# Kernel tuning notes

Hardware: AMD Instinct MI355X
Metric: run time of the kernel (lower is better)

## Reference

```python
import jax, jax.numpy as jnp
import numpy as np

EPS = 1e-5
K = 20
THRESH = 0.5

def _bn_relu(x, g, b, m, v):
    # eval-mode BatchNorm1d followed by ReLU
    return jax.nn.relu(g * (x - m) * jax.lax.rsqrt(v + EPS) + b)

def setup_inputs() -> dict:
    key = jax.random.key(0)
    ks = jax.random.split(key, 16)
    T, C, CI, E, NC = 16384, 256, 8, 5, 13
    B, N = 2, T // 2
    inp = {
        "f_sem": jax.random.normal(ks[0], (T, C), jnp.float32),
        "f_ins": jax.random.normal(ks[1], (T, CI), jnp.float32),
        # equal-size, sorted batch assignment (2 clouds of 8192 points)
        "batch": jnp.repeat(jnp.arange(B, dtype=jnp.int64), N),
        # semantic_adaptation_fc: Linear(C,C) + BN + ReLU
        "W_sem": jax.random.normal(ks[2], (C, C), jnp.float32) * (1.0 / np.sqrt(C)),
        "b_sem": jnp.zeros((C,), jnp.float32),
        "g_sem": jnp.ones((C,), jnp.float32),
        "beta_sem": jnp.zeros((C,), jnp.float32),
        "m_sem": jax.random.normal(ks[3], (C,), jnp.float32) * 0.1,
        "v_sem": jax.random.uniform(ks[4], (C,), jnp.float32, 0.5, 1.5),
        # inst_fc: Linear(8,C) + BN + ReLU
        "W_ins": jax.random.normal(ks[5], (CI, C), jnp.float32) * (1.0 / np.sqrt(CI)),
        "b_ins": jnp.zeros((C,), jnp.float32),
        "g_ins": jnp.ones((C,), jnp.float32),
        "beta_ins": jnp.zeros((C,), jnp.float32),
        "m_ins": jax.random.normal(ks[6], (C,), jnp.float32) * 0.1,
        "v_ins": jax.random.uniform(ks[7], (C,), jnp.float32, 0.5, 1.5),
        # instance_embedding_fc: plain Linear(C,E)
        "W_emb": jax.random.normal(ks[8], (C, E), jnp.float32) * (1.0 / np.sqrt(C)),
        "b_emb": jnp.zeros((E,), jnp.float32),
        # classifier_fc: plain Linear(C,NC)
        "W_cls": jax.random.normal(ks[9], (C, NC), jnp.float32) * (1.0 / np.sqrt(C)),
        "b_cls": jnp.zeros((NC,), jnp.float32),
    }
    return inp

def _instance_fusion(e_ins, f_sem, batch):
    # assumes sorted batch with equal-size segments (enforced by setup_inputs)
    T, C = f_sem.shape
    B = int(batch[-1]) + 1
    N = T // B
    e = e_ins.reshape(B, N, -1)
    f = f_sem.reshape(B, N, C)
    # squared Euclidean pairwise distances per cloud: [B, N, N]
    sq = jnp.sum(e * e, axis=-1)
    d2 = sq[:, :, None] + sq[:, None, :] - 2.0 * jnp.einsum("bnd,bmd->bnm", e, e)
    d2 = jnp.maximum(d2, 0.0)
    neg_vals, idx = jax.lax.top_k(-d2, K)          # k smallest distances, [B,N,K]
    within = (-neg_vals) <= THRESH * THRESH        # distance <= threshold
    self_idx = jnp.broadcast_to(jnp.arange(N)[None, :, None], idx.shape)
    col = jnp.where(within, idx, self_idx)         # fall back to self outside threshold
    neigh = jax.vmap(lambda fb, cb: fb[cb])(f, col)  # [B,N,K,C]
    return jnp.max(neigh, axis=2).reshape(T, C)      # scatter-max == max over neighbors

def reference(f_sem, f_ins, batch,
              W_sem, b_sem, g_sem, beta_sem, m_sem, v_sem,
              W_ins, b_ins, g_ins, beta_ins, m_ins, v_ins,
              W_emb, b_emb, W_cls, b_cls):
    f_sem_prime = _bn_relu(f_sem @ W_sem + b_sem, g_sem, beta_sem, m_sem, v_sem)
    f_ins_h = _bn_relu(f_ins @ W_ins + b_ins, g_ins, beta_ins, m_ins, v_ins)
    f_sins = f_ins_h + f_sem_prime
    e_ins = f_sins @ W_emb + b_emb
    f_isem = _instance_fusion(e_ins, f_sem, batch)
    p_sem = f_isem @ W_cls + b_cls
    return (p_sem, e_ins)
```

## Files before the change

kernel.cpp:

```cpp
#include <hip/hip_runtime.h>
#include <math.h>

#define T 16384
#define C 256
#define CI 8
#define EDIM 5
#define NC 13
#define NPTS 8192
#define KNN 20
#define CAP 192
#define FR 32
#define FRPB 8
#define NCVT 256

typedef float f4v __attribute__((ext_vector_type(4)));
typedef _Float16 h8 __attribute__((ext_vector_type(8)));
typedef _Float16 h4v __attribute__((ext_vector_type(4)));

__global__ __launch_bounds__(256) void front_kernel(
    const float* __restrict__ f_sem, const float* __restrict__ f_ins,
    const float* __restrict__ W_sem, const float* __restrict__ b_sem,
    const float* __restrict__ g_sem, const float* __restrict__ beta_sem,
    const float* __restrict__ m_sem, const float* __restrict__ v_sem,
    const float* __restrict__ W_ins, const float* __restrict__ b_ins,
    const float* __restrict__ g_ins, const float* __restrict__ beta_ins,
    const float* __restrict__ m_ins, const float* __restrict__ v_ins,
    const float* __restrict__ W_emb, const float* __restrict__ b_emb,
    float* __restrict__ eA, double* __restrict__ eD,
    float* __restrict__ out_e, _Float16* __restrict__ fsem_h)
{
    const int nFront = T / FR;
    if (blockIdx.x >= nFront) {
        const size_t total = (size_t)T * C;
        const size_t stride = (size_t)NCVT * 256 * 8;
        size_t i = ((size_t)(blockIdx.x - nFront) * 256 + threadIdx.x) * 8;
        for (; i < total; i += stride) {
            const float4 a = *(const float4*)(f_sem + i);
            const float4 b = *(const float4*)(f_sem + i + 4);
            h8 h;
            h[0] = (_Float16)a.x; h[1] = (_Float16)a.y;
            h[2] = (_Float16)a.z; h[3] = (_Float16)a.w;
            h[4] = (_Float16)b.x; h[5] = (_Float16)b.y;
            h[6] = (_Float16)b.z; h[7] = (_Float16)b.w;
            *(h8*)(fsem_h + i) = h;
        }
        return;
    }

    __shared__ __align__(16) _Float16 sAh[FR][264];
    __shared__ __align__(16) _Float16 sAl[FR][264];
    __shared__ float bnA1[C], bnB1[C], bnA2[C], bnB2[C];
    __shared__ float weL[C][EDIM];
    __shared__ float lfi[FR][CI];
    __shared__ float sP[4][FR][EDIM];

    const int tid = threadIdx.x;
    const int rowBase = blockIdx.x * FR;

    #pragma unroll
    for (int i = 0; i < 8; i++) {
        const int idx = tid + 256 * i;
        const int g = idx * 4;
        const int row = g >> 8, k = g & 255;
        const float4 v = *(const float4*)(f_sem + (size_t)rowBase * C + g);
        const float vv[4] = {v.x, v.y, v.z, v.w};
        #pragma unroll
        for (int q = 0; q < 4; q++) {
            const _Float16 h = (_Float16)vv[q];
            sAh[row][k + q] = h;
            sAl[row][k + q] = (_Float16)(vv[q] - (float)h);
        }
    }
    {
        const int c = tid;
        const float rs1 = 1.0f / sqrtf(v_sem[c] + 1e-5f);
        const float A1 = g_sem[c] * rs1;
        bnA1[c] = A1;
        bnB1[c] = A1 * (b_sem[c] - m_sem[c]) + beta_sem[c];
        const float rs2 = 1.0f / sqrtf(v_ins[c] + 1e-5f);
        const float A2 = g_ins[c] * rs2;
        bnA2[c] = A2;
        bnB2[c] = A2 * (b_ins[c] - m_ins[c]) + beta_ins[c];
        #pragma unroll
        for (int j = 0; j < EDIM; j++) weL[c][j] = W_emb[c * EDIM + j];
    }
    if (tid < FR * CI) lfi[tid >> 3][tid & 7] = f_ins[rowBase * CI + tid];
    __syncthreads();

    const int w = tid >> 6, lane = tid & 63;
    const int r16 = lane & 15, kq = lane >> 4;
    const int n0 = 64 * w;

    f4v acc[2][4];
    #pragma unroll
    for (int mi = 0; mi < 2; mi++)
        #pragma unroll
        for (int ni = 0; ni < 4; ni++) acc[mi][ni] = (f4v){0.f, 0.f, 0.f, 0.f};

    for (int kt = 0; kt < 8; kt++) {
        const int koff = 32 * kt + 8 * kq;
        const h8 ah0 = *(const h8*)&sAh[r16][koff];
        const h8 ah1 = *(const h8*)&sAh[r16 + 16][koff];
        const h8 al0 = *(const h8*)&sAl[r16][koff];
        const h8 al1 = *(const h8*)&sAl[r16 + 16][koff];
        #pragma unroll
        for (int ni = 0; ni < 4; ni++) {
            const float* wp = W_sem + (size_t)koff * C + (n0 + 16 * ni + r16);
            float wf[8];
            #pragma unroll
            for (int j = 0; j < 8; j++) wf[j] = wp[(size_t)j * C];
            h8 bh, bl;
            #pragma unroll
            for (int j = 0; j < 8; j++) {
                const _Float16 h = (_Float16)wf[j];
                bh[j] = h;
                bl[j] = (_Float16)(wf[j] - (float)h);
            }
            acc[0][ni] = __builtin_amdgcn_mfma_f32_16x16x32_f16(ah0, bh, acc[0][ni], 0, 0, 0);
            acc[1][ni] = __builtin_amdgcn_mfma_f32_16x16x32_f16(ah1, bh, acc[1][ni], 0, 0, 0);
            acc[0][ni] = __builtin_amdgcn_mfma_f32_16x16x32_f16(al0, bh, acc[0][ni], 0, 0, 0);
            acc[1][ni] = __builtin_amdgcn_mfma_f32_16x16x32_f16(al1, bh, acc[1][ni], 0, 0, 0);
            acc[0][ni] = __builtin_amdgcn_mfma_f32_16x16x32_f16(ah0, bl, acc[0][ni], 0, 0, 0);
            acc[1][ni] = __builtin_amdgcn_mfma_f32_16x16x32_f16(ah1, bl, acc[1][ni], 0, 0, 0);
        }
    }

    f4v prow, pcol;
    {
        const f4v z = {0.f, 0.f, 0.f, 0.f};
        h8 ra, rb, ca, cb;
        #pragma unroll
        for (int j = 0; j < 8; j++) {
            ra[j] = (_Float16)(float)r16;
            rb[j] = (_Float16)((kq == 0 && j == 0) ? 1.0f : 0.0f);
            ca[j] = rb[j];
            cb[j] = ra[j];
        }
        prow = __builtin_amdgcn_mfma_f32_16x16x32_f16(ra, rb, z, 0, 0, 0);
        pcol = __builtin_amdgcn_mfma_f32_16x16x32_f16(ca, cb, z, 0, 0, 0);
    }
    const int colm = (int)pcol[0];
    int rloc[4];
    #pragma unroll
    for (int r = 0; r < 4; r++) rloc[r] = (int)prow[r];

    float p[2][4][EDIM];
    #pragma unroll
    for (int mi = 0; mi < 2; mi++)
        #pragma unroll
        for (int r = 0; r < 4; r++)
            #pragma unroll
            for (int j = 0; j < EDIM; j++) p[mi][r][j] = 0.f;

    #pragma unroll
    for (int ni = 0; ni < 4; ni++) {
        const int c = n0 + 16 * ni + colm;
        const float A1 = bnA1[c], B1 = bnB1[c];
        const float A2 = bnA2[c], B2 = bnB2[c];
        float wi[CI], we[EDIM];
        #pragma unroll
        for (int k = 0; k < CI; k++) wi[k] = W_ins[k * C + c];
        #pragma unroll
        for (int j = 0; j < EDIM; j++) we[j] = weL[c][j];
        #pragma unroll
        for (int mi = 0; mi < 2; mi++)
            #pragma unroll
            for (int r = 0; r < 4; r++) {
                const int row = 16 * mi + rloc[r];
                float x2 = 0.f;
                #pragma unroll
                for (int k = 0; k < CI; k++) x2 = fmaf(lfi[row][k], wi[k], x2);
                const float h1 = fmaxf(fmaf(A1, acc[mi][ni][r], B1), 0.f);
                const float h2 = fmaxf(fmaf(A2, x2, B2), 0.f);
                const float s = h1 + h2;
                #pragma unroll
                for (int j = 0; j < EDIM; j++) p[mi][r][j] = fmaf(s, we[j], p[mi][r][j]);
            }
    }

    #pragma unroll
    for (int off = 1; off < 16; off <<= 1)
        #pragma unroll
        for (int mi = 0; mi < 2; mi++)
            #pragma unroll
            for (int r = 0; r < 4; r++)
                #pragma unroll
                for (int j = 0; j < EDIM; j++)
                    p[mi][r][j] += __shfl_xor(p[mi][r][j], off);

    if (r16 == 0) {
        #pragma unroll
        for (int mi = 0; mi < 2; mi++)
            #pragma unroll
            for (int r = 0; r < 4; r++)
                #pragma unroll
                for (int j = 0; j < EDIM; j++)
                    sP[w][16 * mi + rloc[r]][j] = p[mi][r][j];
    }
    __syncthreads();

    if (tid < FR) {
        const int row = rowBase + tid;
        double sq = 0.0;
        #pragma unroll
        for (int j = 0; j < EDIM; j++) {
            const float s = ((sP[0][tid][j] + sP[1][tid][j]) +
                             (sP[2][tid][j] + sP[3][tid][j])) + b_emb[j];
            const double ed = (double)s;
            eD[(size_t)row * 8 + j] = ed;
            sq = fma(ed, ed, sq);
            eA[(size_t)row * 8 + j] = s;
            out_e[(size_t)row * EDIM + j] = s;
        }
        eD[(size_t)row * 8 + 5] = sq;
        eA[(size_t)row * 8 + 5] = (float)sq;
        eA[(size_t)row * 8 + 6] = 0.f;
        eA[(size_t)row * 8 + 7] = 0.f;
    }
}

__device__ __attribute__((noinline)) float4 rescan_topk(
    const float* __restrict__ eA, const float* __restrict__ f_sem,
    const float* __restrict__ reRow, int cbase, int lane)
{
    float re0 = reRow[0], re1 = reRow[1], re2 = reRow[2];
    float re3 = reRow[3], re4 = reRow[4], sqF = reRow[5];
    float4 mx = make_float4(-3.4e38f, -3.4e38f, -3.4e38f, -3.4e38f);
    long long last = -1;
    for (int sel = 0; sel < KNN; sel++) {
        long long best = 0x7fffffffffffffffLL;
        for (int cb = 0; cb < NPTS; cb += 64) {
            const int j = cbase + cb + lane;
            const float4 ea = *(const float4*)(eA + (size_t)j * 8);
            const float2 eb = *(const float2*)(eA + (size_t)j * 8 + 4);
            float dot = re0 * ea.x;
            dot = fmaf(re1, ea.y, dot); dot = fmaf(re2, ea.z, dot);
            dot = fmaf(re3, ea.w, dot); dot = fmaf(re4, eb.x, dot);
            const float d2 = fmaxf((sqF + eb.y) - 2.f * dot, 0.f);
            long long key = (((long long)__float_as_uint(d2)) << 32)
                            | (unsigned int)(cb + lane);
            if (key <= last) key = 0x7fffffffffffffffLL;
            if (key < best) best = key;
        }
        #pragma unroll
        for (int off = 32; off; off >>= 1) {
            const long long o = __shfl_xor(best, off);
            if (o < best) best = o;
        }
        last = best;
        const int idx = (int)(best & 0xffffffffLL);
        const float4 fv = *(const float4*)(f_sem + (size_t)(cbase + idx) * C + lane * 4);
        mx.x = fmaxf(mx.x, fv.x); mx.y = fmaxf(mx.y, fv.y);
        mx.z = fmaxf(mx.z, fv.z); mx.w = fmaxf(mx.w, fv.w);
    }
    return mx;
}

template <bool H16>
__global__ __launch_bounds__(256) void knn_kernel(
    const float* __restrict__ eA, const double* __restrict__ eD,
    const float* __restrict__ f_sem, const _Float16* __restrict__ fsem_h,
    const float* __restrict__ W_cls, const float* __restrict__ b_cls,
    float* __restrict__ out_p)
{
    __shared__ float rA[FRPB][8];
    __shared__ double rD[FRPB][6];
    __shared__ unsigned short cidx[FRPB][CAP];
    __shared__ unsigned long long kP[FRPB][CAP];
    __shared__ int cntS[FRPB];
    __shared__ unsigned short memL[FRPB][24];
    __shared__ int nlS[FRPB];

    const int tid = threadIdx.x;
    const int rowBase = blockIdx.x * FRPB;

    if (tid < FRPB * 8) rA[tid >> 3][tid & 7] = eA[(rowBase + (tid >> 3)) * 8 + (tid & 7)];
    if (tid < FRPB * 6) rD[tid / 6][tid % 6] = eD[(rowBase + tid / 6) * 8 + tid % 6];
    if (tid < FRPB) cntS[tid] = 0;
    __syncthreads();

    const int wave = tid >> 6, lane = tid & 63;
    const int cbase = (rowBase >= NPTS) ? NPTS : 0;

    {
        float re[FRPB][5], thrb[FRPB];
        #pragma unroll
        for (int r = 0; r < FRPB; r++) {
            #pragma unroll
            for (int q = 0; q < 5; q++) re[r][q] = rA[r][q];
            thrb[r] = (rA[r][5] - 0.251f) * 0.5f;
        }

        const int cstart = wave * (NPTS / 4);
        for (int cb = cstart; cb < cstart + NPTS / 4; cb += 128) {
            const int j0 = cbase + cb + lane;
            const float4 ea0 = *(const float4*)(eA + (size_t)j0 * 8);
            const float2 eb0 = *(const float2*)(eA + (size_t)j0 * 8 + 4);
            const float4 ea1 = *(const float4*)(eA + (size_t)(j0 + 64) * 8);
            const float2 eb1 = *(const float2*)(eA + (size_t)(j0 + 64) * 8 + 4);
            const float hs0 = 0.5f * eb0.y, hs1 = 0.5f * eb1.y;
            #pragma unroll
            for (int r = 0; r < FRPB; r++) {
                float dot = re[r][0] * ea0.x;
                dot = fmaf(re[r][1], ea0.y, dot); dot = fmaf(re[r][2], ea0.z, dot);
                dot = fmaf(re[r][3], ea0.w, dot); dot = fmaf(re[r][4], eb0.x, dot);
                if (dot >= (thrb[r] + hs0)) {
                    const int pos = atomicAdd(&cntS[r], 1);
                    if (pos < CAP) cidx[r][pos] = (unsigned short)(cb + lane);
                }
            }
            #pragma unroll
            for (int r = 0; r < FRPB; r++) {
                float dot = re[r][0] * ea1.x;
                dot = fmaf(re[r][1], ea1.y, dot); dot = fmaf(re[r][2], ea1.z, dot);
                dot = fmaf(re[r][3], ea1.w, dot); dot = fmaf(re[r][4], eb1.x, dot);
                if (dot >= (thrb[r] + hs1)) {
                    const int pos = atomicAdd(&cntS[r], 1);
                    if (pos < CAP) cidx[r][pos] = (unsigned short)(cb + 64 + lane);
                }
            }
        }
    }
    __syncthreads();

    const int lr0 = 2 * wave, lr1 = lr0 + 1;

    #pragma unroll 1
    for (int rr = 0; rr < 2; rr++) {
        const int lr = lr0 + rr;
        const int cnt = cntS[lr];
        const double* rd = rD[lr];

        if (cnt <= CAP) {
            unsigned long long mykp[4];
            int myid[4], mpos[4];
            bool mem[4];
            #pragma unroll
            for (int q = 0; q < 4; q++) {
                const int i = lane + 64 * q;
                mykp[q] = ~0ull; myid[q] = -1; mem[q] = false;
                if (i < cnt) {
                    const int id = (int)cidx[lr][i];
                    const double* ep = eD + (size_t)(cbase + id) * 8;
                    double dotd = 0.0;
                    #pragma unroll
                    for (int qq = 0; qq < 5; qq++) dotd = fma(rd[qq], ep[qq], dotd);
                    const double d2 = fmax((rd[5] + ep[5]) - 2.0 * dotd, 0.0);
                    if (d2 <= 0.25) {
                        mem[q] = true;
                        const unsigned int k32 = __float_as_uint((float)d2);
                        mykp[q] = (((unsigned long long)k32) << 16) | (unsigned int)id;
                        myid[q] = id;
                    }
                }
            }
            int base = 0;
            #pragma unroll
            for (int q = 0; q < 4; q++) {
                const unsigned long long b = __ballot(mem[q]);
                if (mem[q]) {
                    const int pos = base + (int)__builtin_amdgcn_mbcnt_hi(
                        (unsigned int)(b >> 32),
                        __builtin_amdgcn_mbcnt_lo((unsigned int)b, 0u));
                    mpos[q] = pos;
                    kP[lr][pos] = mykp[q];
                }
                base += (int)__popcll(b);
            }
            const int m = base;

            if (m <= KNN) {
                #pragma unroll
                for (int q = 0; q < 4; q++)
                    if (mem[q]) memL[lr][mpos[q]] = (unsigned short)myid[q];
                if (lane == 0) nlS[lr] = m;
            } else {
                int rank[4] = {0, 0, 0, 0};
                for (int j = 0; j < m; j++) {
                    const unsigned long long kj = kP[lr][j];
                    #pragma unroll
                    for (int q = 0; q < 4; q++) rank[q] += (kj < mykp[q]) ? 1 : 0;
                }
                int sbase = 0;
                #pragma unroll
                for (int q = 0; q < 4; q++) {
                    const bool sel = mem[q] && (rank[q] < KNN);
                    const unsigned long long b = __ballot(sel);
                    if (sel) {
                        const int pos = sbase + (int)__builtin_amdgcn_mbcnt_hi(
                            (unsigned int)(b >> 32),
                            __builtin_amdgcn_mbcnt_lo((unsigned int)b, 0u));
                        memL[lr][pos] = (unsigned short)myid[q];
                    }
                    sbase += (int)__popcll(b);
                }
                if (lane == 0) nlS[lr] = sbase;
            }
        } else {
            if (lane == 0) { memL[lr][0] = 0; nlS[lr] = -1; }
        }
    }

    const int s0 = nlS[lr0], s1 = nlS[lr1];
    const bool fb0 = (s0 < 0), fb1 = (s1 < 0);
    const int n0 = fb0 ? 1 : s0, n1 = fb1 ? 1 : s1;
    float4 mx0 = make_float4(-3.4e38f, -3.4e38f, -3.4e38f, -3.4e38f);
    float4 mx1 = mx0;
    const int nmax = (n0 > n1) ? n0 : n1;

    if (H16) {
        for (int k = 0; k < nmax; k += 8) {
            int a[8], c[8];
            #pragma unroll
            for (int i = 0; i < 8; i++) {
                a[i] = (int)memL[lr0][(k + i < n0) ? k + i : n0 - 1];
                c[i] = (int)memL[lr1][(k + i < n1) ? k + i : n1 - 1];
            }
            h4v fa[8], fc[8];
            #pragma unroll
            for (int i = 0; i < 8; i++) {
                fa[i] = *(const h4v*)(fsem_h + (size_t)(cbase + a[i]) * C + lane * 4);
                fc[i] = *(const h4v*)(fsem_h + (size_t)(cbase + c[i]) * C + lane * 4);
            }
            #pragma unroll
            for (int i = 0; i < 8; i++) {
                mx0.x = fmaxf(mx0.x, (float)fa[i][0]);
                mx0.y = fmaxf(mx0.y, (float)fa[i][1]);
                mx0.z = fmaxf(mx0.z, (float)fa[i][2]);
                mx0.w = fmaxf(mx0.w, (float)fa[i][3]);
                mx1.x = fmaxf(mx1.x, (float)fc[i][0]);
                mx1.y = fmaxf(mx1.y, (float)fc[i][1]);
                mx1.z = fmaxf(mx1.z, (float)fc[i][2]);
                mx1.w = fmaxf(mx1.w, (float)fc[i][3]);
            }
        }
    } else {
        for (int k = 0; k < nmax; k += 4) {
            const int a0 = (int)memL[lr0][(k     < n0) ? k     : n0 - 1];
            const int a1 = (int)memL[lr0][(k + 1 < n0) ? k + 1 : n0 - 1];
            const int a2 = (int)memL[lr0][(k + 2 < n0) ? k + 2 : n0 - 1];
            const int a3 = (int)memL[lr0][(k + 3 < n0) ? k + 3 : n0 - 1];
            const int c0 = (int)memL[lr1][(k     < n1) ? k     : n1 - 1];
            const int c1 = (int)memL[lr1][(k + 1 < n1) ? k + 1 : n1 - 1];
            const int c2 = (int)memL[lr1][(k + 2 < n1) ? k + 2 : n1 - 1];
            const int c3 = (int)memL[lr1][(k + 3 < n1) ? k + 3 : n1 - 1];
            const float4 f0 = *(const float4*)(f_sem + (size_t)(cbase + a0) * C + lane * 4);
            const float4 f1 = *(const float4*)(f_sem + (size_t)(cbase + a1) * C + lane * 4);
            const float4 f2 = *(const float4*)(f_sem + (size_t)(cbase + a2) * C + lane * 4);
            const float4 f3 = *(const float4*)(f_sem + (size_t)(cbase + a3) * C + lane * 4);
            const float4 g0 = *(const float4*)(f_sem + (size_t)(cbase + c0) * C + lane * 4);
            const float4 g1 = *(const float4*)(f_sem + (size_t)(cbase + c1) * C + lane * 4);
            const float4 g2 = *(const float4*)(f_sem + (size_t)(cbase + c2) * C + lane * 4);
            const float4 g3 = *(const float4*)(f_sem + (size_t)(cbase + c3) * C + lane * 4);
            mx0.x = fmaxf(fmaxf(fmaxf(mx0.x, f0.x), fmaxf(f1.x, f2.x)), f3.x);
            mx0.y = fmaxf(fmaxf(fmaxf(mx0.y, f0.y), fmaxf(f1.y, f2.y)), f3.y);
            mx0.z = fmaxf(fmaxf(fmaxf(mx0.z, f0.z), fmaxf(f1.z, f2.z)), f3.z);
            mx0.w = fmaxf(fmaxf(fmaxf(mx0.w, f0.w), fmaxf(f1.w, f2.w)), f3.w);
            mx1.x = fmaxf(fmaxf(fmaxf(mx1.x, g0.x), fmaxf(g1.x, g2.x)), g3.x);
            mx1.y = fmaxf(fmaxf(fmaxf(mx1.y, g0.y), fmaxf(g1.y, g2.y)), g3.y);
            mx1.z = fmaxf(fmaxf(fmaxf(mx1.z, g0.z), fmaxf(g1.z, g2.z)), g3.z);
            mx1.w = fmaxf(fmaxf(fmaxf(mx1.w, g0.w), fmaxf(g1.w, g2.w)), g3.w);
        }
    }
    if (fb0) mx0 = rescan_topk(eA, f_sem, rA[lr0], cbase, lane);
    if (fb1) mx1 = rescan_topk(eA, f_sem, rA[lr1], cbase, lane);

    #pragma unroll 1
    for (int rr = 0; rr < 2; rr++) {
        const float4 mx = rr ? mx1 : mx0;
        float p[NC];
        #pragma unroll
        for (int k = 0; k < NC; k++) p[k] = 0.f;
        const float* w0 = W_cls + (4 * lane + 0) * NC;
        const float* w1 = W_cls + (4 * lane + 1) * NC;
        const float* w2 = W_cls + (4 * lane + 2) * NC;
        const float* w3 = W_cls + (4 * lane + 3) * NC;
        #pragma unroll
        for (int k = 0; k < NC; k++)
            p[k] = fmaf(mx.x, w0[k], fmaf(mx.y, w1[k], fmaf(mx.z, w2[k], fmaf(mx.w, w3[k], p[k]))));
        #pragma unroll
        for (int off = 32; off; off >>= 1)
            #pragma unroll
            for (int k = 0; k < NC; k++) p[k] += __shfl_xor(p[k], off);
        if (lane == 0) {
            const int row = rowBase + lr0 + rr;
            #pragma unroll
            for (int k = 0; k < NC; k++) out_p[row * NC + k] = p[k] + b_cls[k];
        }
    }
}

extern "C" void kernel_launch(void* const* d_in, const int* in_sizes, int n_in,
                              void* d_out, int out_size, void* d_ws, size_t ws_size,
                              hipStream_t stream) {
    (void)in_sizes; (void)n_in; (void)out_size;
    const float* f_sem    = (const float*)d_in[0];
    const float* f_ins    = (const float*)d_in[1];
    const float* W_sem    = (const float*)d_in[3];
    const float* b_sem    = (const float*)d_in[4];
    const float* g_sem    = (const float*)d_in[5];
    const float* beta_sem = (const float*)d_in[6];
    const float* m_sem    = (const float*)d_in[7];
    const float* v_sem    = (const float*)d_in[8];
    const float* W_ins    = (const float*)d_in[9];
    const float* b_ins    = (const float*)d_in[10];
    const float* g_ins    = (const float*)d_in[11];
    const float* beta_ins = (const float*)d_in[12];
    const float* m_ins    = (const float*)d_in[13];
    const float* v_ins    = (const float*)d_in[14];
    const float* W_emb    = (const float*)d_in[15];
    const float* b_emb    = (const float*)d_in[16];
    const float* W_cls    = (const float*)d_in[17];
    const float* b_cls    = (const float*)d_in[18];
    float* outp = (float*)d_out;

    char* ws = (char*)d_ws;
    float*    eA     = (float*)ws;
    double*   eD     = (double*)(ws + (size_t)T * 8 * 4);
    _Float16* fsem_h = (_Float16*)(ws + (size_t)T * 8 * 12);

    const size_t need_h16 = (size_t)T * 8 * 12 + (size_t)T * C * 2;
    const bool h16 = (ws_size >= need_h16);

    const int nFront = T / FR;
    front_kernel<<<h16 ? nFront + NCVT : nFront, 256, 0, stream>>>(
        f_sem, f_ins, W_sem, b_sem, g_sem, beta_sem, m_sem, v_sem,
        W_ins, b_ins, g_ins, beta_ins, m_ins, v_ins, W_emb, b_emb,
        eA, eD, outp + T * NC, h16 ? fsem_h : (_Float16*)nullptr);
    if (h16)
        knn_kernel<true><<<T / FRPB, 256, 0, stream>>>(
            eA, eD, f_sem, fsem_h, W_cls, b_cls, outp);
    else
        knn_kernel<false><<<T / FRPB, 256, 0, stream>>>(
            eA, eD, f_sem, (const _Float16*)nullptr, W_cls, b_cls, outp);
}
```

Before: 170.0 us.

## Compute KNN candidate distances with split-fp16 MFMA and 16 rows per block

The candidate-filter pass now computes squared distances with matrix instructions instead of scalar FMAs. Each embedding is encoded as augmented fp16 hi/lo vectors (query: -2e, |e|^2, 1; key: e, 1, |e|^2), and three 16x16x32 MFMAs per 16-key tile give the full distance. The block now handles 16 query rows, so each key load is shared by twice as many rows, and the front kernel writes the extra encoded arrays. Only a quarter of the lanes feed nonzero K-slices, so much of the MFMA width is unused. The split-fp16 encoding may also shift borderline candidates near the threshold, and CAP arrays were reduced to 3 slots per lane.

```diff
diff --git a/kernel.cpp b/kernel.cpp
--- a/kernel.cpp
+++ b/kernel.cpp
@@ -10,7 +10,7 @@
 #define KNN 20
 #define CAP 192
 #define FR 32
-#define FRPB 8
+#define FRPB 16
 #define NCVT 256
 
 typedef float f4v __attribute__((ext_vector_type(4)));
@@ -27,6 +27,8 @@
     const float* __restrict__ m_ins, const float* __restrict__ v_ins,
     const float* __restrict__ W_emb, const float* __restrict__ b_emb,
     float* __restrict__ eA, double* __restrict__ eD,
+    _Float16* __restrict__ eQh, _Float16* __restrict__ eQl,
+    _Float16* __restrict__ eKh, _Float16* __restrict__ eKl,
     float* __restrict__ out_e, _Float16* __restrict__ fsem_h)
 {
     const int nFront = T / FR;
@@ -202,10 +204,12 @@
     if (tid < FR) {
         const int row = rowBase + tid;
         double sq = 0.0;
+        float ef[EDIM];
         #pragma unroll
         for (int j = 0; j < EDIM; j++) {
             const float s = ((sP[0][tid][j] + sP[1][tid][j]) +
                              (sP[2][tid][j] + sP[3][tid][j])) + b_emb[j];
+            ef[j] = s;
             const double ed = (double)s;
             eD[(size_t)row * 8 + j] = ed;
             sq = fma(ed, ed, sq);
@@ -216,6 +220,23 @@
         eA[(size_t)row * 8 + 5] = (float)sq;
         eA[(size_t)row * 8 + 6] = 0.f;
         eA[(size_t)row * 8 + 7] = 0.f;
+
+        const float sqf = (float)sq;
+        const float qf[8] = {-2.f * ef[0], -2.f * ef[1], -2.f * ef[2],
+                             -2.f * ef[3], -2.f * ef[4], sqf, 1.f, 0.f};
+        const float kf[8] = {ef[0], ef[1], ef[2], ef[3], ef[4], 1.f, sqf, 0.f};
+        h8 qh, ql, kh, kl;
+        #pragma unroll
+        for (int j = 0; j < 8; j++) {
+            const _Float16 hq = (_Float16)qf[j];
+            qh[j] = hq; ql[j] = (_Float16)(qf[j] - (float)hq);
+            const _Float16 hk = (_Float16)kf[j];
+            kh[j] = hk; kl[j] = (_Float16)(kf[j] - (float)hk);
+        }
+        *(h8*)(eQh + (size_t)row * 8) = qh;
+        *(h8*)(eQl + (size_t)row * 8) = ql;
+        *(h8*)(eKh + (size_t)row * 8) = kh;
+        *(h8*)(eKl + (size_t)row * 8) = kl;
     }
 }
 
@@ -259,6 +280,8 @@
 template <bool H16>
 __global__ __launch_bounds__(256) void knn_kernel(
     const float* __restrict__ eA, const double* __restrict__ eD,
+    const _Float16* __restrict__ eQh, const _Float16* __restrict__ eQl,
+    const _Float16* __restrict__ eKh, const _Float16* __restrict__ eKl,
     const float* __restrict__ f_sem, const _Float16* __restrict__ fsem_h,
     const float* __restrict__ W_cls, const float* __restrict__ b_cls,
     float* __restrict__ out_p)
@@ -280,63 +303,74 @@
     __syncthreads();
 
     const int wave = tid >> 6, lane = tid & 63;
+    const int r16 = lane & 15, kq = lane >> 4;
     const int cbase = (rowBase >= NPTS) ? NPTS : 0;
 
+    h8 zero8;
+    #pragma unroll
+    for (int j = 0; j < 8; j++) zero8[j] = (_Float16)0.f;
+
+    f4v prow, pcol;
     {
-        float re[FRPB][5], thrb[FRPB];
-        #pragma unroll
-        for (int r = 0; r < FRPB; r++) {
-            #pragma unroll
-            for (int q = 0; q < 5; q++) re[r][q] = rA[r][q];
-            thrb[r] = (rA[r][5] - 0.251f) * 0.5f;
-        }
-
-        const int cstart = wave * (NPTS / 4);
-        for (int cb = cstart; cb < cstart + NPTS / 4; cb += 128) {
-            const int j0 = cbase + cb + lane;
-            const float4 ea0 = *(const float4*)(eA + (size_t)j0 * 8);
-            const float2 eb0 = *(const float2*)(eA + (size_t)j0 * 8 + 4);
-            const float4 ea1 = *(const float4*)(eA + (size_t)(j0 + 64) * 8);
-            const float2 eb1 = *(const float2*)(eA + (size_t)(j0 + 64) * 8 + 4);
-            const float hs0 = 0.5f * eb0.y, hs1 = 0.5f * eb1.y;
-            #pragma unroll
-            for (int r = 0; r < FRPB; r++) {
-                float dot = re[r][0] * ea0.x;
-                dot = fmaf(re[r][1], ea0.y, dot); dot = fmaf(re[r][2], ea0.z, dot);
-                dot = fmaf(re[r][3], ea0.w, dot); dot = fmaf(re[r][4], eb0.x, dot);
-                if (dot >= (thrb[r] + hs0)) {
-                    const int pos = atomicAdd(&cntS[r], 1);
-                    if (pos < CAP) cidx[r][pos] = (unsigned short)(cb + lane);
-                }
-            }
-            #pragma unroll
-            for (int r = 0; r < FRPB; r++) {
-                float dot = re[r][0] * ea1.x;
-                dot = fmaf(re[r][1], ea1.y, dot); dot = fmaf(re[r][2], ea1.z, dot);
-                dot = fmaf(re[r][3], ea1.w, dot); dot = fmaf(re[r][4], eb1.x, dot);
-                if (dot >= (thrb[r] + hs1)) {
-                    const int pos = atomicAdd(&cntS[r], 1);
-                    if (pos < CAP) cidx[r][pos] = (unsigned short)(cb + 64 + lane);
+        const f4v z = {0.f, 0.f, 0.f, 0.f};
+        h8 ra, rb, ca, cb;
+        #pragma unroll
+        for (int j = 0; j < 8; j++) {
+            ra[j] = (_Float16)(float)r16;
+            rb[j] = (_Float16)((kq == 0 && j == 0) ? 1.0f : 0.0f);
+            ca[j] = rb[j];
+            cb[j] = ra[j];
+        }
+        prow = __builtin_amdgcn_mfma_f32_16x16x32_f16(ra, rb, z, 0, 0, 0);
+        pcol = __builtin_amdgcn_mfma_f32_16x16x32_f16(ca, cb, z, 0, 0, 0);
+    }
+    const int colm = (int)pcol[0];
+    int rloc[4];
+    #pragma unroll
+    for (int r = 0; r < 4; r++) rloc[r] = (int)prow[r];
+
+    {
+        h8 aqh = zero8, aql = zero8;
+        if (kq == 0) {
+            aqh = *(const h8*)(eQh + (size_t)(rowBase + r16) * 8);
+            aql = *(const h8*)(eQl + (size_t)(rowBase + r16) * 8);
+        }
+        const int t0 = wave * (NPTS / 16 / 4);
+        for (int t = t0; t < t0 + NPTS / 16 / 4; ++t) {
+            const int key0 = t * 16;
+            h8 bh = zero8, bl = zero8;
+            if (kq == 0) {
+                bh = *(const h8*)(eKh + (size_t)(cbase + key0 + r16) * 8);
+                bl = *(const h8*)(eKl + (size_t)(cbase + key0 + r16) * 8);
+            }
+            f4v acc = (f4v){0.f, 0.f, 0.f, 0.f};
+            acc = __builtin_amdgcn_mfma_f32_16x16x32_f16(aqh, bh, acc, 0, 0, 0);
+            acc = __builtin_amdgcn_mfma_f32_16x16x32_f16(aql, bh, acc, 0, 0, 0);
+            acc = __builtin_amdgcn_mfma_f32_16x16x32_f16(aqh, bl, acc, 0, 0, 0);
+            #pragma unroll
+            for (int r = 0; r < 4; r++) {
+                if (acc[r] <= 0.251f) {
+                    const int row = rloc[r];
+                    const int pos = atomicAdd(&cntS[row], 1);
+                    if (pos < CAP) cidx[row][pos] = (unsigned short)(key0 + colm);
                 }
             }
         }
     }
     __syncthreads();
 
-    const int lr0 = 2 * wave, lr1 = lr0 + 1;
-
     #pragma unroll 1
-    for (int rr = 0; rr < 2; rr++) {
-        const int lr = lr0 + rr;
+    for (int rr = 0; rr < 4; rr++) {
+        const int lr = 4 * wave + rr;
         const int cnt = cntS[lr];
         const double* rd = rD[lr];
 
         if (cnt <= CAP) {
-            unsigned long long mykp[4];
-            int myid[4], mpos[4];
-            bool mem[4];
-            #pragma unroll
-            for (int q = 0; q < 4; q++) {
+            unsigned long long mykp[3];
+            int myid[3], mpos[3];
+            bool mem[3];
+            #pragma unroll
+            for (int q = 0; q < 3; q++) {
                 const int i = lane + 64 * q;
                 mykp[q] = ~0ull; myid[q] = -1; mem[q] = false;
                 if (i < cnt) {
@@ -356,7 +390,7 @@
             }
             int base = 0;
             #pragma unroll
-            for (int q = 0; q < 4; q++) {
+            for (int q = 0; q < 3; q++) {
                 const unsigned long long b = __ballot(mem[q]);
                 if (mem[q]) {
                     const int pos = base + (int)__builtin_amdgcn_mbcnt_hi(
@@ -371,19 +405,19 @@
 
             if (m <= KNN) {
                 #pragma unroll
-                for (int q = 0; q < 4; q++)
+                for (int q = 0; q < 3; q++)
                     if (mem[q]) memL[lr][mpos[q]] = (unsigned short)myid[q];
                 if (lane == 0) nlS[lr] = m;
             } else {
-                int rank[4] = {0, 0, 0, 0};
+                int rank[3] = {0, 0, 0};
                 for (int j = 0; j < m; j++) {
                     const unsigned long long kj = kP[lr][j];
                     #pragma unroll
-                    for (int q = 0; q < 4; q++) rank[q] += (kj < mykp[q]) ? 1 : 0;
+                    for (int q = 0; q < 3; q++) rank[q] += (kj < mykp[q]) ? 1 : 0;
                 }
                 int sbase = 0;
                 #pragma unroll
-                for (int q = 0; q < 4; q++) {
+                for (int q = 0; q < 3; q++) {
                     const bool sel = mem[q] && (rank[q] < KNN);
                     const unsigned long long b = __ballot(sel);
                     if (sel) {
@@ -401,91 +435,95 @@
         }
     }
 
-    const int s0 = nlS[lr0], s1 = nlS[lr1];
-    const bool fb0 = (s0 < 0), fb1 = (s1 < 0);
-    const int n0 = fb0 ? 1 : s0, n1 = fb1 ? 1 : s1;
-    float4 mx0 = make_float4(-3.4e38f, -3.4e38f, -3.4e38f, -3.4e38f);
-    float4 mx1 = mx0;
-    const int nmax = (n0 > n1) ? n0 : n1;
-
-    if (H16) {
-        for (int k = 0; k < nmax; k += 8) {
-            int a[8], c[8];
-            #pragma unroll
-            for (int i = 0; i < 8; i++) {
-                a[i] = (int)memL[lr0][(k + i < n0) ? k + i : n0 - 1];
-                c[i] = (int)memL[lr1][(k + i < n1) ? k + i : n1 - 1];
-            }
-            h4v fa[8], fc[8];
-            #pragma unroll
-            for (int i = 0; i < 8; i++) {
-                fa[i] = *(const h4v*)(fsem_h + (size_t)(cbase + a[i]) * C + lane * 4);
-                fc[i] = *(const h4v*)(fsem_h + (size_t)(cbase + c[i]) * C + lane * 4);
-            }
-            #pragma unroll
-            for (int i = 0; i < 8; i++) {
-                mx0.x = fmaxf(mx0.x, (float)fa[i][0]);
-                mx0.y = fmaxf(mx0.y, (float)fa[i][1]);
-                mx0.z = fmaxf(mx0.z, (float)fa[i][2]);
-                mx0.w = fmaxf(mx0.w, (float)fa[i][3]);
-                mx1.x = fmaxf(mx1.x, (float)fc[i][0]);
-                mx1.y = fmaxf(mx1.y, (float)fc[i][1]);
-                mx1.z = fmaxf(mx1.z, (float)fc[i][2]);
-                mx1.w = fmaxf(mx1.w, (float)fc[i][3]);
-            }
-        }
-    } else {
-        for (int k = 0; k < nmax; k += 4) {
-            const int a0 = (int)memL[lr0][(k     < n0) ? k     : n0 - 1];
-            const int a1 = (int)memL[lr0][(k + 1 < n0) ? k + 1 : n0 - 1];
-            const int a2 = (int)memL[lr0][(k + 2 < n0) ? k + 2 : n0 - 1];
-            const int a3 = (int)memL[lr0][(k + 3 < n0) ? k + 3 : n0 - 1];
-            const int c0 = (int)memL[lr1][(k     < n1) ? k     : n1 - 1];
-            const int c1 = (int)memL[lr1][(k + 1 < n1) ? k + 1 : n1 - 1];
-            const int c2 = (int)memL[lr1][(k + 2 < n1) ? k + 2 : n1 - 1];
-            const int c3 = (int)memL[lr1][(k + 3 < n1) ? k + 3 : n1 - 1];
-            const float4 f0 = *(const float4*)(f_sem + (size_t)(cbase + a0) * C + lane * 4);
-            const float4 f1 = *(const float4*)(f_sem + (size_t)(cbase + a1) * C + lane * 4);
-            const float4 f2 = *(const float4*)(f_sem + (size_t)(cbase + a2) * C + lane * 4);
-            const float4 f3 = *(const float4*)(f_sem + (size_t)(cbase + a3) * C + lane * 4);
-            const float4 g0 = *(const float4*)(f_sem + (size_t)(cbase + c0) * C + lane * 4);
-            const float4 g1 = *(const float4*)(f_sem + (size_t)(cbase + c1) * C + lane * 4);
-            const float4 g2 = *(const float4*)(f_sem + (size_t)(cbase + c2) * C + lane * 4);
-            const float4 g3 = *(const float4*)(f_sem + (size_t)(cbase + c3) * C + lane * 4);
-            mx0.x = fmaxf(fmaxf(fmaxf(mx0.x, f0.x), fmaxf(f1.x, f2.x)), f3.x);
-            mx0.y = fmaxf(fmaxf(fmaxf(mx0.y, f0.y), fmaxf(f1.y, f2.y)), f3.y);
-            mx0.z = fmaxf(fmaxf(fmaxf(mx0.z, f0.z), fmaxf(f1.z, f2.z)), f3.z);
-            mx0.w = fmaxf(fmaxf(fmaxf(mx0.w, f0.w), fmaxf(f1.w, f2.w)), f3.w);
-            mx1.x = fmaxf(fmaxf(fmaxf(mx1.x, g0.x), fmaxf(g1.x, g2.x)), g3.x);
-            mx1.y = fmaxf(fmaxf(fmaxf(mx1.y, g0.y), fmaxf(g1.y, g2.y)), g3.y);
-            mx1.z = fmaxf(fmaxf(fmaxf(mx1.z, g0.z), fmaxf(g1.z, g2.z)), g3.z);
-            mx1.w = fmaxf(fmaxf(fmaxf(mx1.w, g0.w), fmaxf(g1.w, g2.w)), g3.w);
-        }
-    }
-    if (fb0) mx0 = rescan_topk(eA, f_sem, rA[lr0], cbase, lane);
-    if (fb1) mx1 = rescan_topk(eA, f_sem, rA[lr1], cbase, lane);
-
     #pragma unroll 1
-    for (int rr = 0; rr < 2; rr++) {
-        const float4 mx = rr ? mx1 : mx0;
-        float p[NC];
-        #pragma unroll
-        for (int k = 0; k < NC; k++) p[k] = 0.f;
-        const float* w0 = W_cls + (4 * lane + 0) * NC;
-        const float* w1 = W_cls + (4 * lane + 1) * NC;
-        const float* w2 = W_cls + (4 * lane + 2) * NC;
-        const float* w3 = W_cls + (4 * lane + 3) * NC;
-        #pragma unroll
-        for (int k = 0; k < NC; k++)
-            p[k] = fmaf(mx.x, w0[k], fmaf(mx.y, w1[k], fmaf(mx.z, w2[k], fmaf(mx.w, w3[k], p[k]))));
-        #pragma unroll
-        for (int off = 32; off; off >>= 1)
-            #pragma unroll
-            for (int k = 0; k < NC; k++) p[k] += __shfl_xor(p[k], off);
-        if (lane == 0) {
-            const int row = rowBase + lr0 + rr;
-            #pragma unroll
-            for (int k = 0; k < NC; k++) out_p[row * NC + k] = p[k] + b_cls[k];
+    for (int pp = 0; pp < 2; pp++) {
+        const int lr0 = 4 * wave + 2 * pp, lr1 = lr0 + 1;
+        const int s0 = nlS[lr0], s1 = nlS[lr1];
+        const bool fb0 = (s0 < 0), fb1 = (s1 < 0);
+        const int n0 = fb0 ? 1 : s0, n1 = fb1 ? 1 : s1;
+        float4 mx0 = make_float4(-3.4e38f, -3.4e38f, -3.4e38f, -3.4e38f);
+        float4 mx1 = mx0;
+        const int nmax = (n0 > n1) ? n0 : n1;
+
+        if (H16) {
+            for (int k = 0; k < nmax; k += 8) {
+                int a[8], c[8];
+                #pragma unroll
+                for (int i = 0; i < 8; i++) {
+                    a[i] = (int)memL[lr0][(k + i < n0) ? k + i : n0 - 1];
+                    c[i] = (int)memL[lr1][(k + i < n1) ? k + i : n1 - 1];
+                }
+                h4v fa[8], fc[8];
+                #pragma unroll
+                for (int i = 0; i < 8; i++) {
+                    fa[i] = *(const h4v*)(fsem_h + (size_t)(cbase + a[i]) * C + lane * 4);
+                    fc[i] = *(const h4v*)(fsem_h + (size_t)(cbase + c[i]) * C + lane * 4);
+                }
+                #pragma unroll
+                for (int i = 0; i < 8; i++) {
+                    mx0.x = fmaxf(mx0.x, (float)fa[i][0]);
+                    mx0.y = fmaxf(mx0.y, (float)fa[i][1]);
+                    mx0.z = fmaxf(mx0.z, (float)fa[i][2]);
+                    mx0.w = fmaxf(mx0.w, (float)fa[i][3]);
+                    mx1.x = fmaxf(mx1.x, (float)fc[i][0]);
+                    mx1.y = fmaxf(mx1.y, (float)fc[i][1]);
+                    mx1.z = fmaxf(mx1.z, (float)fc[i][2]);
+                    mx1.w = fmaxf(mx1.w, (float)fc[i][3]);
+                }
+            }
+        } else {
+            for (int k = 0; k < nmax; k += 4) {
+                const int a0 = (int)memL[lr0][(k     < n0) ? k     : n0 - 1];
+                const int a1 = (int)memL[lr0][(k + 1 < n0) ? k + 1 : n0 - 1];
+                const int a2 = (int)memL[lr0][(k + 2 < n0) ? k + 2 : n0 - 1];
+                const int a3 = (int)memL[lr0][(k + 3 < n0) ? k + 3 : n0 - 1];
+                const int c0 = (int)memL[lr1][(k     < n1) ? k     : n1 - 1];
+                const int c1 = (int)memL[lr1][(k + 1 < n1) ? k + 1 : n1 - 1];
+                const int c2 = (int)memL[lr1][(k + 2 < n1) ? k + 2 : n1 - 1];
+                const int c3 = (int)memL[lr1][(k + 3 < n1) ? k + 3 : n1 - 1];
+                const float4 f0 = *(const float4*)(f_sem + (size_t)(cbase + a0) * C + lane * 4);
+                const float4 f1 = *(const float4*)(f_sem + (size_t)(cbase + a1) * C + lane * 4);
+                const float4 f2 = *(const float4*)(f_sem + (size_t)(cbase + a2) * C + lane * 4);
+                const float4 f3 = *(const float4*)(f_sem + (size_t)(cbase + a3) * C + lane * 4);
+                const float4 g0 = *(const float4*)(f_sem + (size_t)(cbase + c0) * C + lane * 4);
+                const float4 g1 = *(const float4*)(f_sem + (size_t)(cbase + c1) * C + lane * 4);
+                const float4 g2 = *(const float4*)(f_sem + (size_t)(cbase + c2) * C + lane * 4);
+                const float4 g3 = *(const float4*)(f_sem + (size_t)(cbase + c3) * C + lane * 4);
+                mx0.x = fmaxf(fmaxf(fmaxf(mx0.x, f0.x), fmaxf(f1.x, f2.x)), f3.x);
+                mx0.y = fmaxf(fmaxf(fmaxf(mx0.y, f0.y), fmaxf(f1.y, f2.y)), f3.y);
+                mx0.z = fmaxf(fmaxf(fmaxf(mx0.z, f0.z), fmaxf(f1.z, f2.z)), f3.z);
+                mx0.w = fmaxf(fmaxf(fmaxf(mx0.w, f0.w), fmaxf(f1.w, f2.w)), f3.w);
+                mx1.x = fmaxf(fmaxf(fmaxf(mx1.x, g0.x), fmaxf(g1.x, g2.x)), g3.x);
+                mx1.y = fmaxf(fmaxf(fmaxf(mx1.y, g0.y), fmaxf(g1.y, g2.y)), g3.y);
+                mx1.z = fmaxf(fmaxf(fmaxf(mx1.z, g0.z), fmaxf(g1.z, g2.z)), g3.z);
+                mx1.w = fmaxf(fmaxf(fmaxf(mx1.w, g0.w), fmaxf(g1.w, g2.w)), g3.w);
+            }
+        }
+        if (fb0) mx0 = rescan_topk(eA, f_sem, rA[lr0], cbase, lane);
+        if (fb1) mx1 = rescan_topk(eA, f_sem, rA[lr1], cbase, lane);
+
+        #pragma unroll 1
+        for (int rr = 0; rr < 2; rr++) {
+            const float4 mx = rr ? mx1 : mx0;
+            float p[NC];
+            #pragma unroll
+            for (int k = 0; k < NC; k++) p[k] = 0.f;
+            const float* w0 = W_cls + (4 * lane + 0) * NC;
+            const float* w1 = W_cls + (4 * lane + 1) * NC;
+            const float* w2 = W_cls + (4 * lane + 2) * NC;
+            const float* w3 = W_cls + (4 * lane + 3) * NC;
+            #pragma unroll
+            for (int k = 0; k < NC; k++)
+                p[k] = fmaf(mx.x, w0[k], fmaf(mx.y, w1[k], fmaf(mx.z, w2[k], fmaf(mx.w, w3[k], p[k]))));
+            #pragma unroll
+            for (int off = 32; off; off >>= 1)
+                #pragma unroll
+                for (int k = 0; k < NC; k++) p[k] += __shfl_xor(p[k], off);
+            if (lane == 0) {
+                const int row = rowBase + lr0 + rr;
+                #pragma unroll
+                for (int k = 0; k < NC; k++) out_p[row * NC + k] = p[k] + b_cls[k];
+            }
         }
     }
 }
@@ -517,20 +555,27 @@
     char* ws = (char*)d_ws;
     float*    eA     = (float*)ws;
     double*   eD     = (double*)(ws + (size_t)T * 8 * 4);
-    _Float16* fsem_h = (_Float16*)(ws + (size_t)T * 8 * 12);
-
-    const size_t need_h16 = (size_t)T * 8 * 12 + (size_t)T * C * 2;
+    _Float16* eQh    = (_Float16*)(ws + (size_t)T * 8 * 12);
+    _Float16* eQl    = eQh + (size_t)T * 8;
+    _Float16* eKh    = eQl + (size_t)T * 8;
+    _Float16* eKl    = eKh + (size_t)T * 8;
+    _Float16* fsem_h = eKl + (size_t)T * 8;
+
+    const size_t base_need = (size_t)T * 8 * 12 + (size_t)T * 8 * 2 * 4;
+    const size_t need_h16  = base_need + (size_t)T * C * 2;
     const bool h16 = (ws_size >= need_h16);
 
     const int nFront = T / FR;
     front_kernel<<<h16 ? nFront + NCVT : nFront, 256, 0, stream>>>(
         f_sem, f_ins, W_sem, b_sem, g_sem, beta_sem, m_sem, v_sem,
         W_ins, b_ins, g_ins, beta_ins, m_ins, v_ins, W_emb, b_emb,
-        eA, eD, outp + T * NC, h16 ? fsem_h : (_Float16*)nullptr);
+        eA, eD, eQh, eQl, eKh, eKl, outp + T * NC,
+        h16 ? fsem_h : (_Float16*)nullptr);
     if (h16)
         knn_kernel<true><<<T / FRPB, 256, 0, stream>>>(
-            eA, eD, f_sem, fsem_h, W_cls, b_cls, outp);
+            eA, eD, eQh, eQl, eKh, eKl, f_sem, fsem_h, W_cls, b_cls, outp);
     else
         knn_kernel<false><<<T / FRPB, 256, 0, stream>>>(
-            eA, eD, f_sem, (const _Float16*)nullptr, W_cls, b_cls, outp);
+            eA, eD, eQh, eQl, eKh, eKl, f_sem, (const _Float16*)nullptr,
+            W_cls, b_cls, outp);
 }
```

Result: slower. 244.3 us (+43.7%).
